# Kernel optimization log

Hardware: AMD Instinct MI355X
Metric: run time of the kernel (lower is better)

Reference implementation:

```python
import jax, jax.numpy as jnp
import numpy as np

V, D = 100000, 512
B, K = 32768, 10


def setup_inputs() -> dict:
    key = jax.random.key(0)
    k1, k2, k3, k4, k5 = jax.random.split(key, 5)
    return {
        "center_ids": jax.random.randint(k1, (B,), 0, V),
        "context_ids": jax.random.randint(k2, (B,), 0, V),
        "neg_context_ids": jax.random.randint(k3, (B, K), 0, V),
        "center_emb": jax.random.normal(k4, (V, D), dtype=jnp.float32) * (1.0 / D),
        "context_emb": jax.random.normal(k5, (V, D), dtype=jnp.float32) * (1.0 / D),
    }


def reference(center_ids, context_ids, neg_context_ids, center_emb, context_emb):
    cv = center_emb[center_ids]            # [B, D]
    ctx = context_emb[context_ids]         # [B, D]
    score = jnp.sum(cv * ctx, axis=1)      # [B]
    score = jnp.clip(score, -10.0, 10.0)
    pos_loss = -jax.nn.log_sigmoid(score)  # [B]
    neg = context_emb[neg_context_ids]     # [B, K, D]
    neg_score = jnp.einsum("bkd,bd->bk", neg, cv)  # [B, K]
    neg_score = jnp.clip(neg_score, -10.0, 10.0)
    neg_loss = -jnp.sum(jax.nn.log_sigmoid(-neg_score), axis=1)  # [B]
    return jnp.mean(pos_loss + neg_loss)
```

## Files before the change

kernel.cpp:

```cpp
#include <hip/hip_runtime.h>
#include <math.h>

#define NB 32768
#define NK 10
#define ND 512
#define WPB 4
#define GRID (NB / WPB)
#define NROW (2 + NK)

__global__ __launch_bounds__(256, 4) void sgns_main(
    const int*   __restrict__ center_ids,
    const int*   __restrict__ context_ids,
    const int*   __restrict__ neg_ids,
    const float* __restrict__ center_emb,
    const float* __restrict__ context_emb,
    float*       __restrict__ partials)
{
    const int tid  = threadIdx.x;
    const int lane = tid & 63;
    const int wave = tid >> 6;
    const int b    = blockIdx.x * WPB + wave;

    const float4* base[NROW];
    base[0] = (const float4*)(center_emb  + (size_t)center_ids[b]  * ND) + 2 * lane;
    base[1] = (const float4*)(context_emb + (size_t)context_ids[b] * ND) + 2 * lane;
#pragma unroll
    for (int k = 0; k < NK; ++k)
        base[2 + k] = (const float4*)(context_emb + (size_t)neg_ids[b * NK + k] * ND) + 2 * lane;

    __builtin_amdgcn_sched_barrier(0);

    float4 r0[NROW], r1[NROW];
#pragma unroll
    for (int i = 0; i < NROW; ++i) {
        r0[i] = base[i][0];
        r1[i] = base[i][1];
    }

    __builtin_amdgcn_sched_barrier(0);

    float part[1 + NK];
#pragma unroll
    for (int i = 0; i < 1 + NK; ++i) {
        const float4 a0 = r0[0], a1 = r1[0];
        const float4 x0 = r0[1 + i], x1 = r1[1 + i];
        part[i] = a0.x * x0.x + a0.y * x0.y + a0.z * x0.z + a0.w * x0.w
                + a1.x * x1.x + a1.y * x1.y + a1.z * x1.z + a1.w * x1.w;
    }

#pragma unroll
    for (int i = 0; i < 1 + NK; ++i) {
        float v = part[i];
#pragma unroll
        for (int off = 32; off > 0; off >>= 1) v += __shfl_xor(v, off, 64);
        part[i] = v;
    }

    float s = fminf(fmaxf(part[0], -10.0f), 10.0f);
    float loss = log1pf(expf(-s));
#pragma unroll
    for (int k = 1; k <= NK; ++k) {
        float t = fminf(fmaxf(part[k], -10.0f), 10.0f);
        loss += log1pf(expf(t));
    }

    __shared__ float ls[WPB];
    if (lane == 0) ls[wave] = loss;
    __syncthreads();
    if (tid == 0)
        partials[blockIdx.x] = ls[0] + ls[1] + ls[2] + ls[3];
}

__global__ __launch_bounds__(1024) void sgns_finish(
    const float* __restrict__ partials, float* __restrict__ out, int n)
{
    __shared__ float ls[1024];
    float s = 0.0f;
    for (int i = threadIdx.x; i < n; i += 1024) s += partials[i];
    ls[threadIdx.x] = s;
    __syncthreads();
    for (int w = 512; w > 0; w >>= 1) {
        if (threadIdx.x < w) ls[threadIdx.x] += ls[threadIdx.x + w];
        __syncthreads();
    }
    if (threadIdx.x == 0) out[0] = ls[0] * (1.0f / (float)NB);
}

extern "C" void kernel_launch(void* const* d_in, const int* in_sizes, int n_in,
                              void* d_out, int out_size, void* d_ws, size_t ws_size,
                              hipStream_t stream) {
    const int*   center_ids  = (const int*)d_in[0];
    const int*   context_ids = (const int*)d_in[1];
    const int*   neg_ids     = (const int*)d_in[2];
    const float* center_emb  = (const float*)d_in[3];
    const float* context_emb = (const float*)d_in[4];
    float* out      = (float*)d_out;
    float* partials = (float*)d_ws;

    sgns_main<<<GRID, 256, 0, stream>>>(center_ids, context_ids, neg_ids,
                                        center_emb, context_emb, partials);
    sgns_finish<<<1, 1024, 0, stream>>>(partials, out, GRID);
}
```

Measured before the change: 125.7 us.

## Split each wave into four 16-lane groups scoring rows in parallel

Each wavefront now splits into four 16-lane groups, and each group computes dot products for one of three row slots per pass. This cuts the cross-lane reduction from 6 to 4 shuffle steps per score, and the cross-lane reductions and transcendentals are evaluated once per group rather than for all 11 scores. The third row batch is loaded after the first score is computed, overlapping its load latency with compute, and the center vector is held in registers for reuse. The slot-12 padding re-fetches the context row and masks it out, which adds a redundant gather. Launch bounds drop to 3 blocks per CU, fast __expf/__logf replace log1pf/expf, and the precision of the result changes slightly.

New measurement: 119.8 us. -4.7%, faster.

```diff
diff --git a/kernel.cpp b/kernel.cpp
--- a/kernel.cpp
+++ b/kernel.cpp
@@ -6,9 +6,8 @@
 #define ND 512
 #define WPB 4
 #define GRID (NB / WPB)
-#define NROW (2 + NK)
 
-__global__ __launch_bounds__(256, 4) void sgns_main(
+__global__ __launch_bounds__(256, 3) void sgns_main(
     const int*   __restrict__ center_ids,
     const int*   __restrict__ context_ids,
     const int*   __restrict__ neg_ids,
@@ -19,53 +18,89 @@
     const int tid  = threadIdx.x;
     const int lane = tid & 63;
     const int wave = tid >> 6;
+    const int grp  = lane >> 4;
+    const int li   = lane & 15;
     const int b    = blockIdx.x * WPB + wave;
 
-    const float4* base[NROW];
-    base[0] = (const float4*)(center_emb  + (size_t)center_ids[b]  * ND) + 2 * lane;
-    base[1] = (const float4*)(context_emb + (size_t)context_ids[b] * ND) + 2 * lane;
+    const int ctx_id = context_ids[b];
+    int rid[3];
 #pragma unroll
-    for (int k = 0; k < NK; ++k)
-        base[2 + k] = (const float4*)(context_emb + (size_t)neg_ids[b * NK + k] * ND) + 2 * lane;
+    for (int r = 0; r < 3; ++r) {
+        const int s = r * 4 + grp;
+        rid[r] = (s == 0 || s == 11) ? ctx_id : neg_ids[b * NK + (s - 1)];
+    }
+
+    const float4* cvp = (const float4*)(center_emb  + (size_t)center_ids[b] * ND) + li;
+    const float4* rpA = (const float4*)(context_emb + (size_t)rid[0] * ND) + li;
+    const float4* rpB = (const float4*)(context_emb + (size_t)rid[1] * ND) + li;
+    const float4* rpC = (const float4*)(context_emb + (size_t)rid[2] * ND) + li;
 
     __builtin_amdgcn_sched_barrier(0);
 
-    float4 r0[NROW], r1[NROW];
+    float4 cv[8], ra[8], rb[8];
 #pragma unroll
-    for (int i = 0; i < NROW; ++i) {
-        r0[i] = base[i][0];
-        r1[i] = base[i][1];
+    for (int j = 0; j < 8; ++j) cv[j] = cvp[16 * j];
+#pragma unroll
+    for (int j = 0; j < 8; ++j) ra[j] = rpA[16 * j];
+#pragma unroll
+    for (int j = 0; j < 8; ++j) rb[j] = rpB[16 * j];
+
+    __builtin_amdgcn_sched_barrier(0);
+
+    float lacc = 0.0f;
+
+    {
+        float p = 0.0f;
+#pragma unroll
+        for (int j = 0; j < 8; ++j)
+            p += cv[j].x * ra[j].x + cv[j].y * ra[j].y
+               + cv[j].z * ra[j].z + cv[j].w * ra[j].w;
+#pragma unroll
+        for (int off = 1; off < 16; off <<= 1) p += __shfl_xor(p, off, 64);
+        float t = fminf(fmaxf(p, -10.0f), 10.0f);
+        const int s = grp;
+        t = (s == 0) ? -t : t;
+        lacc += __logf(1.0f + __expf(t));
     }
 
     __builtin_amdgcn_sched_barrier(0);
 
-    float part[1 + NK];
 #pragma unroll
-    for (int i = 0; i < 1 + NK; ++i) {
-        const float4 a0 = r0[0], a1 = r1[0];
-        const float4 x0 = r0[1 + i], x1 = r1[1 + i];
-        part[i] = a0.x * x0.x + a0.y * x0.y + a0.z * x0.z + a0.w * x0.w
-                + a1.x * x1.x + a1.y * x1.y + a1.z * x1.z + a1.w * x1.w;
+    for (int j = 0; j < 8; ++j) ra[j] = rpC[16 * j];
+
+    __builtin_amdgcn_sched_barrier(0);
+
+    {
+        float p = 0.0f;
+#pragma unroll
+        for (int j = 0; j < 8; ++j)
+            p += cv[j].x * rb[j].x + cv[j].y * rb[j].y
+               + cv[j].z * rb[j].z + cv[j].w * rb[j].w;
+#pragma unroll
+        for (int off = 1; off < 16; off <<= 1) p += __shfl_xor(p, off, 64);
+        float t = fminf(fmaxf(p, -10.0f), 10.0f);
+        lacc += __logf(1.0f + __expf(t));
     }
 
+    {
+        float p = 0.0f;
 #pragma unroll
-    for (int i = 0; i < 1 + NK; ++i) {
-        float v = part[i];
+        for (int j = 0; j < 8; ++j)
+            p += cv[j].x * ra[j].x + cv[j].y * ra[j].y
+               + cv[j].z * ra[j].z + cv[j].w * ra[j].w;
 #pragma unroll
-        for (int off = 32; off > 0; off >>= 1) v += __shfl_xor(v, off, 64);
-        part[i] = v;
+        for (int off = 1; off < 16; off <<= 1) p += __shfl_xor(p, off, 64);
+        float t = fminf(fmaxf(p, -10.0f), 10.0f);
+        float l = __logf(1.0f + __expf(t));
+        const int s = 8 + grp;
+        lacc += (s == 11) ? 0.0f : l;
     }
 
-    float s = fminf(fmaxf(part[0], -10.0f), 10.0f);
-    float loss = log1pf(expf(-s));
-#pragma unroll
-    for (int k = 1; k <= NK; ++k) {
-        float t = fminf(fmaxf(part[k], -10.0f), 10.0f);
-        loss += log1pf(expf(t));
-    }
+    lacc += __shfl_xor(lacc, 16, 64);
+    lacc += __shfl_xor(lacc, 32, 64);
 
     __shared__ float ls[WPB];
-    if (lane == 0) ls[wave] = loss;
+    if (lane == 0) ls[wave] = lacc;
     __syncthreads();
     if (tid == 0)
         partials[blockIdx.x] = ls[0] + ls[1] + ls[2] + ls[3];
```
